# Kernel optimization log

Measured on AMD Instinct MI355X. Metric: run time of the kernel, lower is better.

Reference implementation:

```python
import jax, jax.numpy as jnp
import numpy as np

N_NODES = 100000
N_EDGES = 1600000
D_IN = 64
HIDDEN = 64


def _res_gated_conv(x, Wk, Wq, Wv, Ws, b, src, dst, num_nodes):
    # PyG ResGatedGraphConv: eta_ij = sigmoid(k_i + q_j); out_i = skip(x_i) + sum_j eta_ij * v_j + bias
    k = x @ Wk  # [N, H] keys (applied to target/dst side)
    q = x @ Wq  # [N, H] queries (source side)
    v = x @ Wv  # [N, H] values (source side)
    msg = jax.nn.sigmoid(k[dst] + q[src]) * v[src]  # [E, H] gated messages
    agg = jax.ops.segment_sum(msg, dst, num_segments=num_nodes)  # scatter-add to dst
    return agg + x @ Ws + b


def setup_inputs() -> dict:
    key = jax.random.key(0)
    ks = jax.random.split(key, 16)
    scale_in = 1.0 / np.sqrt(D_IN)
    scale_h = 1.0 / np.sqrt(HIDDEN)

    x = jax.random.normal(ks[0], (N_NODES, D_IN), dtype=jnp.float32)
    edge_index = jax.random.randint(ks[1], (2, N_EDGES), 0, N_NODES, dtype=jnp.int64)

    def w(k, din, dout, s):
        return jax.random.normal(k, (din, dout), dtype=jnp.float32) * s

    inp = {
        "x": x,
        "Wk1": w(ks[2], D_IN, HIDDEN, scale_in),
        "Wq1": w(ks[3], D_IN, HIDDEN, scale_in),
        "Wv1": w(ks[4], D_IN, HIDDEN, scale_in),
        "Ws1": w(ks[5], D_IN, HIDDEN, scale_in),
        "b1": jnp.zeros((HIDDEN,), dtype=jnp.float32),
        "Wl1": w(ks[6], HIDDEN, HIDDEN, scale_h),
        "bl1": jnp.zeros((HIDDEN,), dtype=jnp.float32),
        "Wk2": w(ks[7], HIDDEN, HIDDEN, scale_h),
        "Wq2": w(ks[8], HIDDEN, HIDDEN, scale_h),
        "Wv2": w(ks[9], HIDDEN, HIDDEN, scale_h),
        "Ws2": w(ks[10], HIDDEN, HIDDEN, scale_h),
        "b2": jnp.zeros((HIDDEN,), dtype=jnp.float32),
        "Wl2": w(ks[11], HIDDEN, HIDDEN, scale_h),
        "bl2": jnp.zeros((HIDDEN,), dtype=jnp.float32),
        "edge_index": edge_index,
    }
    return inp


def reference(x, Wk1, Wq1, Wv1, Ws1, b1, Wl1, bl1,
              Wk2, Wq2, Wv2, Ws2, b2, Wl2, bl2, edge_index):
    src, dst = edge_index[0], edge_index[1]
    n = x.shape[0]
    h = _res_gated_conv(x, Wk1, Wq1, Wv1, Ws1, b1, src, dst, n)
    h = jax.nn.relu(h @ Wl1 + bl1)
    h = _res_gated_conv(h, Wk2, Wq2, Wv2, Ws2, b2, src, dst, n)
    h = jax.nn.relu(h @ Wl2 + bl2)
    return h
```

## Files before the change

kernel.cpp:

```cpp
#include <hip/hip_runtime.h>

#define N_NODES 100000
#define N_EDGES 1600000
#define NB      782
#define NBLK_E  256
#define CHUNK_E 6250
#define EBUF_CAP 4096

typedef unsigned short ushort_t;
typedef unsigned int uint_t;

static __device__ __forceinline__ ushort_t bf16_rne(float f) {
    uint_t u = __float_as_uint(f);
    u = (u + 0x7FFFu + ((u >> 16) & 1u)) >> 16;
    return (ushort_t)u;
}
static __device__ __forceinline__ uint_t bfpack(float lo, float hi) {
    return (uint_t)bf16_rne(lo) | ((uint_t)bf16_rne(hi) << 16);
}
static __device__ __forceinline__ float bf2f(ushort_t h) {
    return __uint_as_float(((uint_t)h) << 16);
}

#define FMA16(A, xv) do { \
    A[0]  = fmaf((xv), wa.x, A[0]);  A[1]  = fmaf((xv), wa.y, A[1]);  \
    A[2]  = fmaf((xv), wa.z, A[2]);  A[3]  = fmaf((xv), wa.w, A[3]);  \
    A[4]  = fmaf((xv), wb.x, A[4]);  A[5]  = fmaf((xv), wb.y, A[5]);  \
    A[6]  = fmaf((xv), wb.z, A[6]);  A[7]  = fmaf((xv), wb.w, A[7]);  \
    A[8]  = fmaf((xv), wc.x, A[8]);  A[9]  = fmaf((xv), wc.y, A[9]);  \
    A[10] = fmaf((xv), wc.z, A[10]); A[11] = fmaf((xv), wc.w, A[11]); \
    A[12] = fmaf((xv), wd.x, A[12]); A[13] = fmaf((xv), wd.y, A[13]); \
    A[14] = fmaf((xv), wd.z, A[14]); A[15] = fmaf((xv), wd.w, A[15]); \
} while (0)

__global__ __launch_bounds__(256) void hist782_kernel(
    const int* __restrict__ EI, int* __restrict__ hmat)
{
    __shared__ int h[NB];
    const int tid = threadIdx.x;
    for (int i = tid; i < NB; i += 256) h[i] = 0;
    __syncthreads();
    const int e0 = blockIdx.x * CHUNK_E;
    for (int i = tid; i < CHUNK_E; i += 256) {
        int d = EI[N_EDGES + e0 + i];
        atomicAdd(&h[d >> 7], 1);
    }
    __syncthreads();
    int* row = hmat + blockIdx.x * NB;
    for (int i = tid; i < NB; i += 256) row[i] = h[i];
}

__global__ __launch_bounds__(1024) void colscan_kernel(
    int* __restrict__ hmat, int* __restrict__ bbase2, int* __restrict__ btot)
{
    __shared__ int s[1024];
    const int tid = threadIdx.x;
    int run = 0;
    if (tid < NB) {
        for (int blk = 0; blk < NBLK_E; ++blk) {
            int idx = blk * NB + tid;
            int v = hmat[idx];
            hmat[idx] = run;
            run += v;
        }
    }
    s[tid] = (tid < NB) ? run : 0;
    __syncthreads();
    for (int off = 1; off < 1024; off <<= 1) {
        int t = (tid >= off) ? s[tid - off] : 0;
        __syncthreads();
        s[tid] += t;
        __syncthreads();
    }
    if (tid < NB) {
        bbase2[tid] = s[tid] - run;
        btot[tid]   = run;
    }
}

__global__ __launch_bounds__(256) void scat782_kernel(
    const int* __restrict__ EI, const int* __restrict__ hmat,
    const int* __restrict__ bbase2, uint_t* __restrict__ sbuf)
{
    __shared__ int base[NB];
    __shared__ int cur[NB];
    const int tid = threadIdx.x;
    const int* row = hmat + blockIdx.x * NB;
    for (int i = tid; i < NB; i += 256) {
        base[i] = bbase2[i] + row[i];
        cur[i] = 0;
    }
    __syncthreads();
    const int e0 = blockIdx.x * CHUNK_E;
    for (int i = tid; i < CHUNK_E; i += 256) {
        int sN = EI[e0 + i];
        int d  = EI[N_EDGES + e0 + i];
        int b  = d >> 7;
        int p  = base[b] + atomicAdd(&cur[b], 1);
        sbuf[p] = (uint_t)sN | ((uint_t)(d & 127) << 17);
    }
}

__global__ __launch_bounds__(256) void csr_kernel(
    const int* __restrict__ bbase2, const int* __restrict__ btot,
    const uint_t* __restrict__ sbuf,
    int* __restrict__ deg, int* __restrict__ start, int* __restrict__ ssrc)
{
    __shared__ uint_t ebuf[EBUF_CAP];
    __shared__ int cnt[128];
    __shared__ int lst[128];
    const int b = blockIdx.x, tid = threadIdx.x;
    const int base = bbase2[b];
    int total = btot[b];
    if (total > EBUF_CAP) total = EBUF_CAP;

    if (tid < 128) cnt[tid] = 0;
    __syncthreads();

    for (int i = tid; i < total; i += 256) {
        uint_t u = sbuf[base + i];
        ebuf[i] = u;
        atomicAdd(&cnt[(u >> 17) & 127], 1);
    }
    __syncthreads();

    if (tid < 128) lst[tid] = cnt[tid];
    __syncthreads();
    for (int off = 1; off < 128; off <<= 1) {
        int t = (tid < 128 && tid >= off) ? lst[tid - off] : 0;
        __syncthreads();
        if (tid < 128) lst[tid] += t;
        __syncthreads();
    }
    if (tid < 128) {
        lst[tid] -= cnt[tid];
        int n = b * 128 + tid;
        deg[n] = cnt[tid];
        start[n] = base + lst[tid];
        cnt[tid] = 0;
    }
    __syncthreads();

    for (int i = tid; i < total; i += 256) {
        uint_t u = ebuf[i];
        int dl = (u >> 17) & 127;
        int pos = base + lst[dl] + atomicAdd(&cnt[dl], 1);
        ssrc[pos] = (int)(u & 0x1FFFFu);
    }
}

__global__ __launch_bounds__(256) void transform4_kernel(
    const float* __restrict__ X,
    const float* __restrict__ W0, const float* __restrict__ W1,
    const float* __restrict__ W2, const float* __restrict__ W3,
    const float* __restrict__ B3,
    float* __restrict__ Ek, ushort_t* __restrict__ Eqh,
    ushort_t* __restrict__ Vh, float* __restrict__ AGG)
{
    __shared__ float xs[64][65];
    __shared__ float ws[2][64][64];
    const int tid  = threadIdx.x;
    const int base = blockIdx.x * 64;
    const int pair = blockIdx.y;

    {
        const float* WA = pair ? W2 : W0;
        const float* WB = pair ? W3 : W1;
        float4* dA = (float4*)&ws[0][0][0];
        float4* dB = (float4*)&ws[1][0][0];
        for (int i = tid; i < 1024; i += 256) {
            dA[i] = ((const float4*)WA)[i];
            dB[i] = ((const float4*)WB)[i];
        }
    }
    for (int i = tid; i < 1024; i += 256) {
        int r = i >> 4, c = i & 15;
        int node = base + r;
        float4 v = make_float4(0.f, 0.f, 0.f, 0.f);
        if (node < N_NODES) v = ((const float4*)X)[(size_t)node * 16 + c];
        *(float4*)&xs[r][c * 4] = v;
    }
    __syncthreads();

    const int wid    = tid >> 6;
    const int lane   = tid & 63;
    const int matsel = wid >> 1;
    const int lg     = ((wid & 1) << 6) | lane;
    const int ng     = lg >> 2;
    const int og     = (lg & 3) * 16;

    float acc0[16], acc1[16];
    #pragma unroll
    for (int j = 0; j < 16; ++j) { acc0[j] = 0.f; acc1[j] = 0.f; }

    for (int k = 0; k < 64; ++k) {
        float4 wa = *(const float4*)&ws[matsel][k][og + 0];
        float4 wb = *(const float4*)&ws[matsel][k][og + 4];
        float4 wc = *(const float4*)&ws[matsel][k][og + 8];
        float4 wd = *(const float4*)&ws[matsel][k][og + 12];
        float x0 = xs[2 * ng + 0][k];
        float x1 = xs[2 * ng + 1][k];
        FMA16(acc0, x0);
        FMA16(acc1, x1);
    }

    const int kind = pair * 2 + matsel;
    if (kind == 0) {
        #pragma unroll
        for (int i = 0; i < 2; ++i) {
            int node = base + 2 * ng + i;
            if (node < N_NODES) {
                float* dst = Ek + (size_t)node * 64 + og;
                const float* A = (i == 0) ? acc0 : acc1;
                float e[16];
                #pragma unroll
                for (int j = 0; j < 16; ++j) e[j] = __expf(-A[j]);
                *(float4*)(dst + 0)  = make_float4(e[0],  e[1],  e[2],  e[3]);
                *(float4*)(dst + 4)  = make_float4(e[4],  e[5],  e[6],  e[7]);
                *(float4*)(dst + 8)  = make_float4(e[8],  e[9],  e[10], e[11]);
                *(float4*)(dst + 12) = make_float4(e[12], e[13], e[14], e[15]);
            }
        }
    } else if (kind == 3) {
        float bias[16];
        #pragma unroll
        for (int j = 0; j < 16; ++j) bias[j] = B3[og + j];
        #pragma unroll
        for (int i = 0; i < 2; ++i) {
            int node = base + 2 * ng + i;
            if (node < N_NODES) {
                float* dst = AGG + (size_t)node * 64 + og;
                const float* A = (i == 0) ? acc0 : acc1;
                *(float4*)(dst + 0)  = make_float4(A[0]  + bias[0],  A[1]  + bias[1],
                                                   A[2]  + bias[2],  A[3]  + bias[3]);
                *(float4*)(dst + 4)  = make_float4(A[4]  + bias[4],  A[5]  + bias[5],
                                                   A[6]  + bias[6],  A[7]  + bias[7]);
                *(float4*)(dst + 8)  = make_float4(A[8]  + bias[8],  A[9]  + bias[9],
                                                   A[10] + bias[10], A[11] + bias[11]);
                *(float4*)(dst + 12) = make_float4(A[12] + bias[12], A[13] + bias[13],
                                                   A[14] + bias[14], A[15] + bias[15]);
            }
        }
    } else {
        ushort_t* O = (kind == 1) ? Eqh : Vh;
        const bool doexp = (kind == 1);
        #pragma unroll
        for (int i = 0; i < 2; ++i) {
            int node = base + 2 * ng + i;
            if (node < N_NODES) {
                uint_t* dst = (uint_t*)(O + (size_t)node * 64 + og);
                const float* Araw = (i == 0) ? acc0 : acc1;
                float A[16];
                #pragma unroll
                for (int j = 0; j < 16; ++j)
                    A[j] = doexp ? __expf(-Araw[j]) : Araw[j];
                uint4 u0, u1;
                u0.x = bfpack(A[0],  A[1]);  u0.y = bfpack(A[2],  A[3]);
                u0.z = bfpack(A[4],  A[5]);  u0.w = bfpack(A[6],  A[7]);
                u1.x = bfpack(A[8],  A[9]);  u1.y = bfpack(A[10], A[11]);
                u1.z = bfpack(A[12], A[13]); u1.w = bfpack(A[14], A[15]);
                *(uint4*)(dst + 0) = u0;
                *(uint4*)(dst + 4) = u1;
            }
        }
    }
}

__global__ __launch_bounds__(256) void agg_kernel(
    const float* __restrict__ Ek, const ushort_t* __restrict__ Eqh,
    const ushort_t* __restrict__ Vh, const int* __restrict__ start,
    const int* __restrict__ deg, const int* __restrict__ ssrc,
    float* __restrict__ AGG)
{
    int n = (blockIdx.x * 256 + threadIdx.x) >> 6;
    int lane = threadIdx.x & 63;
    int eg = lane >> 4;
    int c  = (lane & 15) * 4;

    const float4 ekv = *(const float4*)(Ek + (size_t)n * 64 + c);
    float4 acc = make_float4(0.f, 0.f, 0.f, 0.f);

    int s0 = start[n];
    int dn = deg[n];
    for (int p = eg; p < dn; p += 4) {
        int s = ssrc[s0 + p];
        ushort4 qh = *(const ushort4*)(Eqh + (size_t)s * 64 + c);
        ushort4 vh = *(const ushort4*)(Vh + (size_t)s * 64 + c);
        float tx = fmaf(ekv.x, bf2f(qh.x), 1.f);
        float ty = fmaf(ekv.y, bf2f(qh.y), 1.f);
        float tz = fmaf(ekv.z, bf2f(qh.z), 1.f);
        float tw = fmaf(ekv.w, bf2f(qh.w), 1.f);
        acc.x = fmaf(bf2f(vh.x), __builtin_amdgcn_rcpf(tx), acc.x);
        acc.y = fmaf(bf2f(vh.y), __builtin_amdgcn_rcpf(ty), acc.y);
        acc.z = fmaf(bf2f(vh.z), __builtin_amdgcn_rcpf(tz), acc.z);
        acc.w = fmaf(bf2f(vh.w), __builtin_amdgcn_rcpf(tw), acc.w);
    }

    acc.x += __shfl_xor(acc.x, 16); acc.y += __shfl_xor(acc.y, 16);
    acc.z += __shfl_xor(acc.z, 16); acc.w += __shfl_xor(acc.w, 16);
    acc.x += __shfl_xor(acc.x, 32); acc.y += __shfl_xor(acc.y, 32);
    acc.z += __shfl_xor(acc.z, 32); acc.w += __shfl_xor(acc.w, 32);

    if (eg == 0) {
        float4* a = (float4*)(AGG + (size_t)n * 64 + c);
        float4 o = *a;
        o.x += acc.x; o.y += acc.y; o.z += acc.z; o.w += acc.w;
        *a = o;
    }
}

__global__ __launch_bounds__(256) void relu_gemm_kernel(
    const float* __restrict__ AGG, const float* __restrict__ WL,
    const float* __restrict__ BL, float* __restrict__ OUT)
{
    __shared__ float xin[64][65];
    __shared__ float wl[64][64];
    const int tid  = threadIdx.x;
    const int base = blockIdx.x * 64;

    {
        float4* dl = (float4*)&wl[0][0];
        for (int i = tid; i < 1024; i += 256) dl[i] = ((const float4*)WL)[i];
    }
    for (int i = tid; i < 1024; i += 256) {
        int r = i >> 4, c = i & 15;
        int node = base + r;
        float4 v = make_float4(0.f, 0.f, 0.f, 0.f);
        if (node < N_NODES) v = ((const float4*)AGG)[(size_t)node * 16 + c];
        *(float4*)&xin[r][c * 4] = v;
    }
    __syncthreads();

    const int node = tid >> 2;
    const int og   = (tid & 3) * 16;
    float acc[16];
    #pragma unroll
    for (int j = 0; j < 16; ++j) acc[j] = 0.f;
    for (int k = 0; k < 64; ++k) {
        float4 wa = *(const float4*)&wl[k][og + 0];
        float4 wb = *(const float4*)&wl[k][og + 4];
        float4 wc = *(const float4*)&wl[k][og + 8];
        float4 wd = *(const float4*)&wl[k][og + 12];
        float xv = xin[node][k];
        FMA16(acc, xv);
    }

    int out_node = base + node;
    if (out_node < N_NODES) {
        float* dst = OUT + (size_t)out_node * 64 + og;
        float r0[16];
        #pragma unroll
        for (int j = 0; j < 16; ++j) r0[j] = fmaxf(acc[j] + BL[og + j], 0.f);
        *(float4*)(dst + 0)  = make_float4(r0[0],  r0[1],  r0[2],  r0[3]);
        *(float4*)(dst + 4)  = make_float4(r0[4],  r0[5],  r0[6],  r0[7]);
        *(float4*)(dst + 8)  = make_float4(r0[8],  r0[9],  r0[10], r0[11]);
        *(float4*)(dst + 12) = make_float4(r0[12], r0[13], r0[14], r0[15]);
    }
}

extern "C" void kernel_launch(void* const* d_in, const int* in_sizes, int n_in,
                              void* d_out, int out_size, void* d_ws, size_t ws_size,
                              hipStream_t stream)
{
    const float* x   = (const float*)d_in[0];
    const float* Wk1 = (const float*)d_in[1];
    const float* Wq1 = (const float*)d_in[2];
    const float* Wv1 = (const float*)d_in[3];
    const float* Ws1 = (const float*)d_in[4];
    const float* b1  = (const float*)d_in[5];
    const float* Wl1 = (const float*)d_in[6];
    const float* bl1 = (const float*)d_in[7];
    const float* Wk2 = (const float*)d_in[8];
    const float* Wq2 = (const float*)d_in[9];
    const float* Wv2 = (const float*)d_in[10];
    const float* Ws2 = (const float*)d_in[11];
    const float* b2  = (const float*)d_in[12];
    const float* Wl2 = (const float*)d_in[13];
    const float* bl2 = (const float*)d_in[14];
    const int*   ei  = (const int*)d_in[15];

    const size_t NF = (size_t)N_NODES * 64;
    float*    Ek    = (float*)d_ws;
    float*    AGG   = Ek + NF;
    float*    H     = AGG + NF;
    ushort_t* Eqh   = (ushort_t*)(H + NF);
    ushort_t* Vh    = Eqh + NF;
    int*      hmat  = (int*)(Vh + NF);
    int*      bbase2 = hmat + NBLK_E * NB;
    int*      btot  = bbase2 + 1024;
    int*      deg   = btot + 1024;
    int*      start = deg + 100352;
    int*      ssrc  = start + 100352;
    uint_t*   sbuf  = (uint_t*)(ssrc + N_EDGES);

    hist782_kernel<<<NBLK_E, 256, 0, stream>>>(ei, hmat);
    colscan_kernel<<<1, 1024, 0, stream>>>(hmat, bbase2, btot);
    scat782_kernel<<<NBLK_E, 256, 0, stream>>>(ei, hmat, bbase2, sbuf);
    csr_kernel<<<NB, 256, 0, stream>>>(bbase2, btot, sbuf, deg, start, ssrc);

    transform4_kernel<<<dim3(1563, 2), 256, 0, stream>>>(x, Wk1, Wq1, Wv1, Ws1, b1,
                                                         Ek, Eqh, Vh, AGG);
    agg_kernel<<<N_NODES / 4, 256, 0, stream>>>(Ek, Eqh, Vh, start, deg, ssrc, AGG);
    relu_gemm_kernel<<<1563, 256, 0, stream>>>(AGG, Wl1, bl1, H);

    transform4_kernel<<<dim3(1563, 2), 256, 0, stream>>>(H, Wk2, Wq2, Wv2, Ws2, b2,
                                                         Ek, Eqh, Vh, AGG);
    agg_kernel<<<N_NODES / 4, 256, 0, stream>>>(Ek, Eqh, Vh, start, deg, ssrc, AGG);
    relu_gemm_kernel<<<1563, 256, 0, stream>>>(AGG, Wl2, bl2, (float*)d_out);
}
```

Measured before the change: 468.3 us.

## Parallelize bucket column scan, store exp(-k) as bf16, widen agg loads

```diff
diff --git a/kernel.cpp b/kernel.cpp
--- a/kernel.cpp
+++ b/kernel.cpp
@@ -20,6 +20,10 @@
 }
 static __device__ __forceinline__ float bf2f(ushort_t h) {
     return __uint_as_float(((uint_t)h) << 16);
+}
+static __device__ __forceinline__ void bf2x2(uint_t u, float& lo, float& hi) {
+    lo = __uint_as_float(u << 16);
+    hi = __uint_as_float(u & 0xFFFF0000u);
 }
 
 #define FMA16(A, xv) do { \
@@ -34,7 +38,7 @@
 } while (0)
 
 __global__ __launch_bounds__(256) void hist782_kernel(
-    const int* __restrict__ EI, int* __restrict__ hmat)
+    const int* __restrict__ EI, int* __restrict__ hmat_t)
 {
     __shared__ int h[NB];
     const int tid = threadIdx.x;
@@ -46,25 +50,41 @@
         atomicAdd(&h[d >> 7], 1);
     }
     __syncthreads();
-    int* row = hmat + blockIdx.x * NB;
-    for (int i = tid; i < NB; i += 256) row[i] = h[i];
-}
-
-__global__ __launch_bounds__(1024) void colscan_kernel(
-    int* __restrict__ hmat, int* __restrict__ bbase2, int* __restrict__ btot)
+    for (int i = tid; i < NB; i += 256)
+        hmat_t[i * NBLK_E + blockIdx.x] = h[i];
+}
+
+__global__ __launch_bounds__(256) void colscan_p1_kernel(
+    int* __restrict__ hmat_t, int* __restrict__ btot)
+{
+    const int b = blockIdx.x * 4 + (threadIdx.x >> 6);
+    if (b >= NB) return;
+    const int lane = threadIdx.x & 63;
+    int4 v = ((int4*)(hmat_t + b * NBLK_E))[lane];
+    const int tot = v.x + v.y + v.z + v.w;
+    int x = tot;
+    #pragma unroll
+    for (int off = 1; off < 64; off <<= 1) {
+        int t = __shfl_up(x, off);
+        if (lane >= off) x += t;
+    }
+    const int base = x - tot;
+    int4 o;
+    o.x = base;
+    o.y = base + v.x;
+    o.z = base + v.x + v.y;
+    o.w = base + v.x + v.y + v.z;
+    ((int4*)(hmat_t + b * NBLK_E))[lane] = o;
+    if (lane == 63) btot[b] = x;
+}
+
+__global__ __launch_bounds__(1024) void colscan_p2_kernel(
+    const int* __restrict__ btot, int* __restrict__ bbase2)
 {
     __shared__ int s[1024];
     const int tid = threadIdx.x;
-    int run = 0;
-    if (tid < NB) {
-        for (int blk = 0; blk < NBLK_E; ++blk) {
-            int idx = blk * NB + tid;
-            int v = hmat[idx];
-            hmat[idx] = run;
-            run += v;
-        }
-    }
-    s[tid] = (tid < NB) ? run : 0;
+    int v = (tid < NB) ? btot[tid] : 0;
+    s[tid] = v;
     __syncthreads();
     for (int off = 1; off < 1024; off <<= 1) {
         int t = (tid >= off) ? s[tid - off] : 0;
@@ -72,22 +92,18 @@
         s[tid] += t;
         __syncthreads();
     }
-    if (tid < NB) {
-        bbase2[tid] = s[tid] - run;
-        btot[tid]   = run;
-    }
+    if (tid < NB) bbase2[tid] = s[tid] - v;
 }
 
 __global__ __launch_bounds__(256) void scat782_kernel(
-    const int* __restrict__ EI, const int* __restrict__ hmat,
+    const int* __restrict__ EI, const int* __restrict__ hmat_t,
     const int* __restrict__ bbase2, uint_t* __restrict__ sbuf)
 {
     __shared__ int base[NB];
     __shared__ int cur[NB];
     const int tid = threadIdx.x;
-    const int* row = hmat + blockIdx.x * NB;
     for (int i = tid; i < NB; i += 256) {
-        base[i] = bbase2[i] + row[i];
+        base[i] = bbase2[i] + hmat_t[i * NBLK_E + blockIdx.x];
         cur[i] = 0;
     }
     __syncthreads();
@@ -154,7 +170,7 @@
     const float* __restrict__ W0, const float* __restrict__ W1,
     const float* __restrict__ W2, const float* __restrict__ W3,
     const float* __restrict__ B3,
-    float* __restrict__ Ek, ushort_t* __restrict__ Eqh,
+    ushort_t* __restrict__ Ekh, ushort_t* __restrict__ Eqh,
     ushort_t* __restrict__ Vh, float* __restrict__ AGG)
 {
     __shared__ float xs[64][65];
@@ -205,23 +221,7 @@
     }
 
     const int kind = pair * 2 + matsel;
-    if (kind == 0) {
-        #pragma unroll
-        for (int i = 0; i < 2; ++i) {
-            int node = base + 2 * ng + i;
-            if (node < N_NODES) {
-                float* dst = Ek + (size_t)node * 64 + og;
-                const float* A = (i == 0) ? acc0 : acc1;
-                float e[16];
-                #pragma unroll
-                for (int j = 0; j < 16; ++j) e[j] = __expf(-A[j]);
-                *(float4*)(dst + 0)  = make_float4(e[0],  e[1],  e[2],  e[3]);
-                *(float4*)(dst + 4)  = make_float4(e[4],  e[5],  e[6],  e[7]);
-                *(float4*)(dst + 8)  = make_float4(e[8],  e[9],  e[10], e[11]);
-                *(float4*)(dst + 12) = make_float4(e[12], e[13], e[14], e[15]);
-            }
-        }
-    } else if (kind == 3) {
+    if (kind == 3) {
         float bias[16];
         #pragma unroll
         for (int j = 0; j < 16; ++j) bias[j] = B3[og + j];
@@ -242,8 +242,8 @@
             }
         }
     } else {
-        ushort_t* O = (kind == 1) ? Eqh : Vh;
-        const bool doexp = (kind == 1);
+        ushort_t* O = (kind == 0) ? Ekh : (kind == 1) ? Eqh : Vh;
+        const bool doexp = (kind < 2);
         #pragma unroll
         for (int i = 0; i < 2; ++i) {
             int node = base + 2 * ng + i;
@@ -267,45 +267,58 @@
 }
 
 __global__ __launch_bounds__(256) void agg_kernel(
-    const float* __restrict__ Ek, const ushort_t* __restrict__ Eqh,
+    const ushort_t* __restrict__ Ekh, const ushort_t* __restrict__ Eqh,
     const ushort_t* __restrict__ Vh, const int* __restrict__ start,
     const int* __restrict__ deg, const int* __restrict__ ssrc,
     float* __restrict__ AGG)
 {
     int n = (blockIdx.x * 256 + threadIdx.x) >> 6;
     int lane = threadIdx.x & 63;
-    int eg = lane >> 4;
-    int c  = (lane & 15) * 4;
-
-    const float4 ekv = *(const float4*)(Ek + (size_t)n * 64 + c);
-    float4 acc = make_float4(0.f, 0.f, 0.f, 0.f);
+    int eg = lane >> 3;
+    int c8 = (lane & 7) * 8;
+
+    uint4 eku = *(const uint4*)(Ekh + (size_t)n * 64 + c8);
+    float ek[8];
+    bf2x2(eku.x, ek[0], ek[1]); bf2x2(eku.y, ek[2], ek[3]);
+    bf2x2(eku.z, ek[4], ek[5]); bf2x2(eku.w, ek[6], ek[7]);
+
+    float acc[8];
+    #pragma unroll
+    for (int j = 0; j < 8; ++j) acc[j] = 0.f;
 
     int s0 = start[n];
     int dn = deg[n];
-    for (int p = eg; p < dn; p += 4) {
+    for (int p = eg; p < dn; p += 8) {
         int s = ssrc[s0 + p];
-        ushort4 qh = *(const ushort4*)(Eqh + (size_t)s * 64 + c);
-        ushort4 vh = *(const ushort4*)(Vh + (size_t)s * 64 + c);
-        float tx = fmaf(ekv.x, bf2f(qh.x), 1.f);
-        float ty = fmaf(ekv.y, bf2f(qh.y), 1.f);
-        float tz = fmaf(ekv.z, bf2f(qh.z), 1.f);
-        float tw = fmaf(ekv.w, bf2f(qh.w), 1.f);
-        acc.x = fmaf(bf2f(vh.x), __builtin_amdgcn_rcpf(tx), acc.x);
-        acc.y = fmaf(bf2f(vh.y), __builtin_amdgcn_rcpf(ty), acc.y);
-        acc.z = fmaf(bf2f(vh.z), __builtin_amdgcn_rcpf(tz), acc.z);
-        acc.w = fmaf(bf2f(vh.w), __builtin_amdgcn_rcpf(tw), acc.w);
-    }
-
-    acc.x += __shfl_xor(acc.x, 16); acc.y += __shfl_xor(acc.y, 16);
-    acc.z += __shfl_xor(acc.z, 16); acc.w += __shfl_xor(acc.w, 16);
-    acc.x += __shfl_xor(acc.x, 32); acc.y += __shfl_xor(acc.y, 32);
-    acc.z += __shfl_xor(acc.z, 32); acc.w += __shfl_xor(acc.w, 32);
+        uint4 qu = *(const uint4*)(Eqh + (size_t)s * 64 + c8);
+        uint4 vu = *(const uint4*)(Vh  + (size_t)s * 64 + c8);
+        float q[8], v[8];
+        bf2x2(qu.x, q[0], q[1]); bf2x2(qu.y, q[2], q[3]);
+        bf2x2(qu.z, q[4], q[5]); bf2x2(qu.w, q[6], q[7]);
+        bf2x2(vu.x, v[0], v[1]); bf2x2(vu.y, v[2], v[3]);
+        bf2x2(vu.z, v[4], v[5]); bf2x2(vu.w, v[6], v[7]);
+        #pragma unroll
+        for (int j = 0; j < 8; ++j) {
+            float t = fmaf(ek[j], q[j], 1.f);
+            acc[j] = fmaf(v[j], __builtin_amdgcn_rcpf(t), acc[j]);
+        }
+    }
+
+    #pragma unroll
+    for (int j = 0; j < 8; ++j) {
+        acc[j] += __shfl_xor(acc[j], 8);
+        acc[j] += __shfl_xor(acc[j], 16);
+        acc[j] += __shfl_xor(acc[j], 32);
+    }
 
     if (eg == 0) {
-        float4* a = (float4*)(AGG + (size_t)n * 64 + c);
-        float4 o = *a;
-        o.x += acc.x; o.y += acc.y; o.z += acc.z; o.w += acc.w;
-        *a = o;
+        float* a = AGG + (size_t)n * 64 + c8;
+        float4 o0 = *(float4*)(a + 0);
+        float4 o1 = *(float4*)(a + 4);
+        o0.x += acc[0]; o0.y += acc[1]; o0.z += acc[2]; o0.w += acc[3];
+        o1.x += acc[4]; o1.y += acc[5]; o1.z += acc[6]; o1.w += acc[7];
+        *(float4*)(a + 0) = o0;
+        *(float4*)(a + 4) = o1;
     }
 }
 
@@ -380,31 +393,32 @@
     const int*   ei  = (const int*)d_in[15];
 
     const size_t NF = (size_t)N_NODES * 64;
-    float*    Ek    = (float*)d_ws;
-    float*    AGG   = Ek + NF;
+    float*    AGG   = (float*)d_ws;
     float*    H     = AGG + NF;
-    ushort_t* Eqh   = (ushort_t*)(H + NF);
+    ushort_t* Ekh   = (ushort_t*)(H + NF);
+    ushort_t* Eqh   = Ekh + NF;
     ushort_t* Vh    = Eqh + NF;
-    int*      hmat  = (int*)(Vh + NF);
-    int*      bbase2 = hmat + NBLK_E * NB;
-    int*      btot  = bbase2 + 1024;
-    int*      deg   = btot + 1024;
-    int*      start = deg + 100352;
-    int*      ssrc  = start + 100352;
-    uint_t*   sbuf  = (uint_t*)(ssrc + N_EDGES);
-
-    hist782_kernel<<<NBLK_E, 256, 0, stream>>>(ei, hmat);
-    colscan_kernel<<<1, 1024, 0, stream>>>(hmat, bbase2, btot);
-    scat782_kernel<<<NBLK_E, 256, 0, stream>>>(ei, hmat, bbase2, sbuf);
+    int*      hmat_t = (int*)(Vh + NF);
+    int*      btot   = hmat_t + NB * NBLK_E;
+    int*      bbase2 = btot + 1024;
+    int*      deg    = bbase2 + 1024;
+    int*      start  = deg + 100352;
+    int*      ssrc   = start + 100352;
+    uint_t*   sbuf   = (uint_t*)(ssrc + N_EDGES);
+
+    hist782_kernel<<<NBLK_E, 256, 0, stream>>>(ei, hmat_t);
+    colscan_p1_kernel<<<(NB + 3) / 4, 256, 0, stream>>>(hmat_t, btot);
+    colscan_p2_kernel<<<1, 1024, 0, stream>>>(btot, bbase2);
+    scat782_kernel<<<NBLK_E, 256, 0, stream>>>(ei, hmat_t, bbase2, sbuf);
     csr_kernel<<<NB, 256, 0, stream>>>(bbase2, btot, sbuf, deg, start, ssrc);
 
     transform4_kernel<<<dim3(1563, 2), 256, 0, stream>>>(x, Wk1, Wq1, Wv1, Ws1, b1,
-                                                         Ek, Eqh, Vh, AGG);
-    agg_kernel<<<N_NODES / 4, 256, 0, stream>>>(Ek, Eqh, Vh, start, deg, ssrc, AGG);
+                                                         Ekh, Eqh, Vh, AGG);
+    agg_kernel<<<N_NODES / 4, 256, 0, stream>>>(Ekh, Eqh, Vh, start, deg, ssrc, AGG);
     relu_gemm_kernel<<<1563, 256, 0, stream>>>(AGG, Wl1, bl1, H);
 
     transform4_kernel<<<dim3(1563, 2), 256, 0, stream>>>(H, Wk2, Wq2, Wv2, Ws2, b2,
-                                                         Ek, Eqh, Vh, AGG);
-    agg_kernel<<<N_NODES / 4, 256, 0, stream>>>(Ek, Eqh, Vh, start, deg, ssrc, AGG);
+                                                         Ekh, Eqh, Vh, AGG);
+    agg_kernel<<<N_NODES / 4, 256, 0, stream>>>(Ekh, Eqh, Vh, start, deg, ssrc, AGG);
     relu_gemm_kernel<<<1563, 256, 0, stream>>>(AGG, Wl2, bl2, (float*)d_out);
 }
```

Result: faster. 438.0 us (-6.5%).
